# Kernel tuning notes

Hardware: AMD Instinct MI355X
Metric: run time of the kernel (lower is better)

The kernel has to match this reference:

```python
import jax, jax.numpy as jnp
import numpy as np
import math

INPUT_SIZE = 512
HIDDEN_SIZE = 1024
B, T = 64, 512


def setup_inputs() -> dict:
    key = jax.random.key(0)
    ks = jax.random.split(key, 8)
    stdv = 1.0 / math.sqrt(HIDDEN_SIZE)
    def U(k, shape):
        return jax.random.uniform(k, shape, jnp.float32, -stdv, stdv)
    x = jax.random.normal(ks[0], (B, T, INPUT_SIZE), jnp.float32)
    W_i_r = U(ks[1], (HIDDEN_SIZE, INPUT_SIZE))
    W_h_r = U(ks[2], (HIDDEN_SIZE, HIDDEN_SIZE))
    W_i_z = U(ks[3], (HIDDEN_SIZE, INPUT_SIZE))
    W_h_z = U(ks[4], (HIDDEN_SIZE, HIDDEN_SIZE))
    W_i_n = U(ks[5], (HIDDEN_SIZE, INPUT_SIZE))
    W_h_n = U(ks[6], (HIDDEN_SIZE, HIDDEN_SIZE))
    zeros = jnp.zeros((HIDDEN_SIZE,), jnp.float32)
    return {
        "x": x,
        "W_i_r": W_i_r, "b_i_r": zeros, "W_h_r": W_h_r, "b_h_r": zeros,
        "W_i_z": W_i_z, "b_i_z": zeros, "W_h_z": W_h_z, "b_h_z": zeros,
        "W_i_n": W_i_n, "b_i_n": zeros, "W_h_n": W_h_n, "b_h_n": zeros,
    }


def reference(x, W_i_r, b_i_r, W_h_r, b_h_r, W_i_z, b_i_z, W_h_z, b_h_z,
              W_i_n, b_i_n, W_h_n, b_h_n):
    Bn, Tn, _ = x.shape
    # Precompute all input projections in one batched matmul each: [B,T,H]
    xr = jnp.einsum('bti,hi->bth', x, W_i_r) + b_i_r
    xz = jnp.einsum('bti,hi->bth', x, W_i_z) + b_i_z
    xn = jnp.einsum('bti,hi->bth', x, W_i_n) + b_i_n

    h0 = jnp.zeros((Bn, W_h_r.shape[0]), x.dtype)

    def step(h, inp):
        xr_t, xz_t, xn_t = inp  # each [B,H]
        r = jax.nn.sigmoid(xr_t + h @ W_h_r.T + b_h_r)
        z = jax.nn.sigmoid(xz_t + h @ W_h_z.T + b_h_z)
        n = jnp.tanh(xn_t + r * (h @ W_h_n.T + b_h_n))
        h_new = (1.0 - z) * n + z * h
        return h_new, h_new

    # scan over time: inputs transposed to [T,B,H]
    xs = (xr.transpose(1, 0, 2), xz.transpose(1, 0, 2), xn.transpose(1, 0, 2))
    _, h_seq = jax.lax.scan(step, h0, xs)
    return h_seq.transpose(1, 0, 2)  # [B,T,H]
```

## Files before the change

### kernel.cpp

```cpp
#include <hip/hip_runtime.h>
#include <math.h>


#define BB 64
#define TT 512
#define II 512
#define HH 1024
#define JB 4
#define CK 128
#define PAD 132
#define XJ 16

__device__ __forceinline__ void fma4(float4& a, const float4 xv, const float4 w) {
    a.x += xv.x * w.x;
    a.y += xv.y * w.y;
    a.z += xv.z * w.z;
    a.w += xv.w * w.w;
}

__global__ __launch_bounds__(256) void xproj(
    const float* __restrict__ x,
    const float* __restrict__ Wir, const float* __restrict__ Wiz,
    const float* __restrict__ Win, float* __restrict__ xpre)
{
    __shared__ float xs[BB][PAD];
    const int tid  = threadIdx.x;
    const int b    = tid & 63;
    const int w    = tid >> 6;
    const int bid  = (int)blockIdx.x;
    const int t    = bid >> 6;
    const int jgrp = bid & 63;
    const int j0   = __builtin_amdgcn_readfirstlane(jgrp * XJ + w * 4);

    float4 acc[4][3];
#pragma unroll
    for (int jj = 0; jj < 4; ++jj)
#pragma unroll
        for (int g = 0; g < 3; ++g)
            acc[jj][g] = {0.f, 0.f, 0.f, 0.f};

    const float* xbase = x + (size_t)t * II;
    for (int kc = 0; kc < II / CK; ++kc) {
#pragma unroll
        for (int i = 0; i < 8; ++i) {
            int f   = tid + 256 * i;
            int row = f >> 5;
            int c4  = f & 31;
            *(float4*)&xs[row][c4 * 4] =
                *(const float4*)(xbase + (size_t)row * (TT * II) + kc * CK + c4 * 4);
        }
        __syncthreads();
        const float* xsrow = &xs[b][0];
#pragma unroll
        for (int k4 = 0; k4 < CK / 4; ++k4) {
            float4 xv = *(const float4*)(xsrow + k4 * 4);
#pragma unroll
            for (int jj = 0; jj < 4; ++jj) {
                const size_t wof = (size_t)(j0 + jj) * II + kc * CK + k4 * 4;
                fma4(acc[jj][0], xv, *(const float4*)(Wir + wof));
                fma4(acc[jj][1], xv, *(const float4*)(Wiz + wof));
                fma4(acc[jj][2], xv, *(const float4*)(Win + wof));
            }
        }
        __syncthreads();
    }

#pragma unroll
    for (int jj = 0; jj < 4; ++jj) {
        const int j = j0 + jj;
#pragma unroll
        for (int g = 0; g < 3; ++g) {
            float s = acc[jj][g].x + acc[jj][g].y + acc[jj][g].z + acc[jj][g].w;
            xpre[(((size_t)g * TT + t) * HH + j) * BB + b] = s;
        }
    }
}

__global__ __launch_bounds__(256) void gru_step_h(
    const float* __restrict__ Whr, const float* __restrict__ Whz,
    const float* __restrict__ Whn,
    const float* __restrict__ bir, const float* __restrict__ bhr,
    const float* __restrict__ biz, const float* __restrict__ bhz,
    const float* __restrict__ bin_, const float* __restrict__ bhn,
    const float* __restrict__ xpre,
    float* __restrict__ out, int t)
{
    __shared__ float xs[BB][PAD];
    const int tid = threadIdx.x;
    const int b   = tid & 63;
    const int jg  = tid >> 6;
    const int j   = __builtin_amdgcn_readfirstlane((int)blockIdx.x * JB + jg);

    const float bir_j = bir[j], bhr_j = bhr[j];
    const float biz_j = biz[j], bhz_j = bhz[j];
    const float bin_j = bin_[j], bhn_j = bhn[j];
    const float xr  = xpre[(((size_t)0 * TT + t) * HH + j) * BB + b];
    const float xz  = xpre[(((size_t)1 * TT + t) * HH + j) * BB + b];
    const float xn0 = xpre[(((size_t)2 * TT + t) * HH + j) * BB + b];
    float hprev = 0.f;
    if (t > 0)
        hprev = out[(size_t)b * (TT * HH) + (size_t)(t - 1) * HH + j];

    float4 aR  = {0.f, 0.f, 0.f, 0.f};
    float4 aZ  = {0.f, 0.f, 0.f, 0.f};
    float4 aHN = {0.f, 0.f, 0.f, 0.f};

    if (t > 0) {
        const float* hbase = out + (size_t)(t - 1) * HH;
        for (int kc = 0; kc < HH / CK; ++kc) {
#pragma unroll
            for (int i = 0; i < 8; ++i) {
                int f   = tid + 256 * i;
                int row = f >> 5;
                int c4  = f & 31;
                *(float4*)&xs[row][c4 * 4] =
                    *(const float4*)(hbase + (size_t)row * (TT * HH) + kc * CK + c4 * 4);
            }
            __syncthreads();
            const float* xsrow = &xs[b][0];
            const float* wr = Whr + (size_t)j * HH + kc * CK;
            const float* wz = Whz + (size_t)j * HH + kc * CK;
            const float* wn = Whn + (size_t)j * HH + kc * CK;
#pragma unroll
            for (int k4 = 0; k4 < CK / 4; ++k4) {
                float4 xv = *(const float4*)(xsrow + k4 * 4);
                fma4(aR,  xv, *(const float4*)(wr + k4 * 4));
                fma4(aZ,  xv, *(const float4*)(wz + k4 * 4));
                fma4(aHN, xv, *(const float4*)(wn + k4 * 4));
            }
            __syncthreads();
        }
    }

    float rpre = (aR.x + aR.y + aR.z + aR.w) + xr + bir_j + bhr_j;
    float zpre = (aZ.x + aZ.y + aZ.z + aZ.w) + xz + biz_j + bhz_j;
    float hn   = (aHN.x + aHN.y + aHN.z + aHN.w) + bhn_j;
    float xn   = xn0 + bin_j;

    float r = 1.f / (1.f + __expf(-rpre));
    float z = 1.f / (1.f + __expf(-zpre));
    float n = tanhf(xn + r * hn);

    out[(size_t)b * (TT * HH) + (size_t)t * HH + j] = (1.f - z) * n + z * hprev;
}

__device__ __forceinline__ void accum_chunk(
    const float* __restrict__ xsrow,
    const float* __restrict__ wr, const float* __restrict__ wz,
    const float* __restrict__ wn,
    float4& aR, float4& aZ, float4& aN)
{
#pragma unroll
    for (int k4 = 0; k4 < CK / 4; ++k4) {
        float4 xv = *(const float4*)(xsrow + k4 * 4);
        fma4(aR, xv, *(const float4*)(wr + k4 * 4));
        fma4(aZ, xv, *(const float4*)(wz + k4 * 4));
        fma4(aN, xv, *(const float4*)(wn + k4 * 4));
    }
}

__global__ __launch_bounds__(256) void gru_step_full(
    const float* __restrict__ x,
    const float* __restrict__ Wir, const float* __restrict__ Whr,
    const float* __restrict__ Wiz, const float* __restrict__ Whz,
    const float* __restrict__ Win, const float* __restrict__ Whn,
    const float* __restrict__ bir, const float* __restrict__ bhr,
    const float* __restrict__ biz, const float* __restrict__ bhz,
    const float* __restrict__ bin_, const float* __restrict__ bhn,
    float* __restrict__ out, int t)
{
    __shared__ float xs[BB][PAD];
    const int tid = threadIdx.x;
    const int b   = tid & 63;
    const int jg  = tid >> 6;
    const int j   = __builtin_amdgcn_readfirstlane((int)blockIdx.x * JB + jg);

    float4 aR  = {0.f, 0.f, 0.f, 0.f};
    float4 aZ  = {0.f, 0.f, 0.f, 0.f};
    float4 aXN = {0.f, 0.f, 0.f, 0.f};
    float4 aHN = {0.f, 0.f, 0.f, 0.f};

    const float* xbase = x + (size_t)t * II;
    for (int kc = 0; kc < II / CK; ++kc) {
#pragma unroll
        for (int i = 0; i < 8; ++i) {
            int f   = tid + 256 * i;
            int row = f >> 5;
            int c4  = f & 31;
            *(float4*)&xs[row][c4 * 4] =
                *(const float4*)(xbase + (size_t)row * (TT * II) + kc * CK + c4 * 4);
        }
        __syncthreads();
        accum_chunk(&xs[b][0],
                    Wir + (size_t)j * II + kc * CK,
                    Wiz + (size_t)j * II + kc * CK,
                    Win + (size_t)j * II + kc * CK,
                    aR, aZ, aXN);
        __syncthreads();
    }

    if (t > 0) {
        const float* hbase = out + (size_t)(t - 1) * HH;
        for (int kc = 0; kc < HH / CK; ++kc) {
#pragma unroll
            for (int i = 0; i < 8; ++i) {
                int f   = tid + 256 * i;
                int row = f >> 5;
                int c4  = f & 31;
                *(float4*)&xs[row][c4 * 4] =
                    *(const float4*)(hbase + (size_t)row * (TT * HH) + kc * CK + c4 * 4);
            }
            __syncthreads();
            accum_chunk(&xs[b][0],
                        Whr + (size_t)j * HH + kc * CK,
                        Whz + (size_t)j * HH + kc * CK,
                        Whn + (size_t)j * HH + kc * CK,
                        aR, aZ, aHN);
            __syncthreads();
        }
    }

    float rpre = (aR.x + aR.y + aR.z + aR.w) + bir[j] + bhr[j];
    float zpre = (aZ.x + aZ.y + aZ.z + aZ.w) + biz[j] + bhz[j];
    float hn   = (aHN.x + aHN.y + aHN.z + aHN.w) + bhn[j];
    float xn   = (aXN.x + aXN.y + aXN.z + aXN.w) + bin_[j];

    float r = 1.f / (1.f + __expf(-rpre));
    float z = 1.f / (1.f + __expf(-zpre));
    float n = tanhf(xn + r * hn);

    float hprev = (t > 0) ? out[(size_t)b * (TT * HH) + (size_t)(t - 1) * HH + j] : 0.f;
    out[(size_t)b * (TT * HH) + (size_t)t * HH + j] = (1.f - z) * n + z * hprev;
}

extern "C" void kernel_launch(void* const* d_in, const int* in_sizes, int n_in,
                              void* d_out, int out_size, void* d_ws, size_t ws_size,
                              hipStream_t stream) {
    (void)in_sizes; (void)n_in; (void)out_size;

    const float* x    = (const float*)d_in[0];
    const float* Wir  = (const float*)d_in[1];
    const float* bir  = (const float*)d_in[2];
    const float* Whr  = (const float*)d_in[3];
    const float* bhr  = (const float*)d_in[4];
    const float* Wiz  = (const float*)d_in[5];
    const float* biz  = (const float*)d_in[6];
    const float* Whz  = (const float*)d_in[7];
    const float* bhz  = (const float*)d_in[8];
    const float* Win  = (const float*)d_in[9];
    const float* bin_ = (const float*)d_in[10];
    const float* Whn  = (const float*)d_in[11];
    const float* bhn  = (const float*)d_in[12];
    float* out = (float*)d_out;

    const size_t need = (size_t)3 * TT * HH * BB * sizeof(float);
    if (d_ws != nullptr && ws_size >= need) {
        float* xpre = (float*)d_ws;
        xproj<<<dim3(TT * 64), dim3(256), 0, stream>>>(x, Wir, Wiz, Win, xpre);
        for (int t = 0; t < TT; ++t) {
            gru_step_h<<<dim3(HH / JB), dim3(256), 0, stream>>>(
                Whr, Whz, Whn, bir, bhr, biz, bhz, bin_, bhn, xpre, out, t);
        }
    } else {
        for (int t = 0; t < TT; ++t) {
            gru_step_full<<<dim3(HH / JB), dim3(256), 0, stream>>>(
                x, Wir, Whr, Wiz, Whz, Win, Whn,
                bir, bhr, biz, bhz, bin_, bhn, out, t);
        }
    }
}
```

Before: 15.86 ms.

## Replace per-timestep kernel launches with a persistent cooperative GRU kernel

Replaces the 512 per-timestep launches of gru_step_h with one cooperative persistent kernel of 256 blocks. Each block loops over time, keeps its biases in registers, reads the previous hidden state from a double-buffered packed global array, and synchronises all blocks through an atomic counter grid barrier after each step. This removes per-step kernel launch overhead. In exchange it adds the cost of a global barrier per step and relies on all blocks being co-resident; if the cooperative launch fails it falls back to the per-step launches.

Result: slower. 38.30 ms (+141.5%).

```diff
diff --git a/kernel.cpp b/kernel.cpp
--- a/kernel.cpp
+++ b/kernel.cpp
@@ -73,6 +73,103 @@
             float s = acc[jj][g].x + acc[jj][g].y + acc[jj][g].z + acc[jj][g].w;
             xpre[(((size_t)g * TT + t) * HH + j) * BB + b] = s;
         }
+    }
+}
+
+__global__ __launch_bounds__(256) void gru_persist(
+    const float* __restrict__ Whr, const float* __restrict__ Whz,
+    const float* __restrict__ Whn,
+    const float* __restrict__ bir, const float* __restrict__ bhr,
+    const float* __restrict__ biz, const float* __restrict__ bhz,
+    const float* __restrict__ bin_, const float* __restrict__ bhn,
+    const float* __restrict__ xpre,
+    float* __restrict__ out, float* __restrict__ hpack,
+    unsigned* __restrict__ bar)
+{
+    __shared__ float hs[CK * BB];
+    const int tid = threadIdx.x;
+    const int b   = tid & 63;
+    const int jg  = tid >> 6;
+    const int j   = __builtin_amdgcn_readfirstlane((int)blockIdx.x * JB + jg);
+
+    const float bir_j = bir[j], bhr_j = bhr[j];
+    const float biz_j = biz[j], bhz_j = bhz[j];
+    const float bin_j = bin_[j], bhn_j = bhn[j];
+
+    const size_t HB = (size_t)HH * BB;
+
+    for (int t = 0; t < TT; ++t) {
+        const float* hp_prev = hpack + (size_t)((t + 1) & 1) * HB;
+        float*       hp_cur  = hpack + (size_t)(t & 1) * HB;
+
+        const float xr  = xpre[(((size_t)0 * TT + t) * HH + j) * BB + b];
+        const float xz  = xpre[(((size_t)1 * TT + t) * HH + j) * BB + b];
+        const float xn0 = xpre[(((size_t)2 * TT + t) * HH + j) * BB + b];
+
+        float4 aR  = {0.f, 0.f, 0.f, 0.f};
+        float4 aZ  = {0.f, 0.f, 0.f, 0.f};
+        float4 aHN = {0.f, 0.f, 0.f, 0.f};
+        float hprev = 0.f;
+
+        if (t > 0) {
+            hprev = hp_prev[(size_t)j * BB + b];
+#pragma unroll 1
+            for (int kc = 0; kc < HH / CK; ++kc) {
+                const float* src = hp_prev + (size_t)kc * (CK * BB);
+#pragma unroll
+                for (int i = 0; i < 8; ++i) {
+                    const int f = tid + 256 * i;
+                    *(float4*)&hs[f * 4] = *(const float4*)(src + (size_t)f * 4);
+                }
+                __syncthreads();
+                const float* wr = Whr + (size_t)j * HH + kc * CK;
+                const float* wz = Whz + (size_t)j * HH + kc * CK;
+                const float* wn = Whn + (size_t)j * HH + kc * CK;
+#pragma unroll
+                for (int k4 = 0; k4 < CK / 4; ++k4) {
+                    const float4 wrv = *(const float4*)(wr + k4 * 4);
+                    const float4 wzv = *(const float4*)(wz + k4 * 4);
+                    const float4 wnv = *(const float4*)(wn + k4 * 4);
+                    const float h0 = hs[(k4 * 4 + 0) * 64 + b];
+                    const float h1 = hs[(k4 * 4 + 1) * 64 + b];
+                    const float h2 = hs[(k4 * 4 + 2) * 64 + b];
+                    const float h3 = hs[(k4 * 4 + 3) * 64 + b];
+                    aR.x  += h0 * wrv.x; aR.y  += h1 * wrv.y;
+                    aR.z  += h2 * wrv.z; aR.w  += h3 * wrv.w;
+                    aZ.x  += h0 * wzv.x; aZ.y  += h1 * wzv.y;
+                    aZ.z  += h2 * wzv.z; aZ.w  += h3 * wzv.w;
+                    aHN.x += h0 * wnv.x; aHN.y += h1 * wnv.y;
+                    aHN.z += h2 * wnv.z; aHN.w += h3 * wnv.w;
+                }
+                __syncthreads();
+            }
+        }
+
+        float rpre = (aR.x + aR.y + aR.z + aR.w) + xr + bir_j + bhr_j;
+        float zpre = (aZ.x + aZ.y + aZ.z + aZ.w) + xz + biz_j + bhz_j;
+        float hn   = (aHN.x + aHN.y + aHN.z + aHN.w) + bhn_j;
+        float xn   = xn0 + bin_j;
+
+        float r = 1.f / (1.f + __expf(-rpre));
+        float z = 1.f / (1.f + __expf(-zpre));
+        float n = tanhf(xn + r * hn);
+        float hnew = (1.f - z) * n + z * hprev;
+
+        out[(size_t)b * (TT * HH) + (size_t)t * HH + j] = hnew;
+        hp_cur[(size_t)j * BB + b] = hnew;
+
+        __syncthreads();
+        if (tid == 0) {
+            __threadfence();
+            __hip_atomic_fetch_add(bar, 1u, __ATOMIC_RELAXED,
+                                   __HIP_MEMORY_SCOPE_AGENT);
+            const unsigned tgt = 256u * (unsigned)(t + 1);
+            while (__hip_atomic_load(bar, __ATOMIC_RELAXED,
+                                     __HIP_MEMORY_SCOPE_AGENT) < tgt)
+                __builtin_amdgcn_s_sleep(2);
+            __threadfence();
+        }
+        __syncthreads();
     }
 }
 
@@ -253,13 +350,30 @@
     const float* bhn  = (const float*)d_in[12];
     float* out = (float*)d_out;
 
-    const size_t need = (size_t)3 * TT * HH * BB * sizeof(float);
+    const size_t XPRE_BYTES  = (size_t)3 * TT * HH * BB * sizeof(float);
+    const size_t HPACK_BYTES = (size_t)2 * HH * BB * sizeof(float);
+    const size_t need = XPRE_BYTES + HPACK_BYTES + 256;
+
     if (d_ws != nullptr && ws_size >= need) {
-        float* xpre = (float*)d_ws;
+        float*    xpre  = (float*)d_ws;
+        float*    hpack = (float*)((char*)d_ws + XPRE_BYTES);
+        unsigned* bar   = (unsigned*)((char*)d_ws + XPRE_BYTES + HPACK_BYTES);
+
+        hipMemsetAsync(bar, 0, 64, stream);
         xproj<<<dim3(TT * 64), dim3(256), 0, stream>>>(x, Wir, Wiz, Win, xpre);
-        for (int t = 0; t < TT; ++t) {
-            gru_step_h<<<dim3(HH / JB), dim3(256), 0, stream>>>(
-                Whr, Whz, Whn, bir, bhr, biz, bhz, bin_, bhn, xpre, out, t);
+
+        void* args[] = { (void*)&Whr, (void*)&Whz, (void*)&Whn,
+                         (void*)&bir, (void*)&bhr, (void*)&biz, (void*)&bhz,
+                         (void*)&bin_, (void*)&bhn, (void*)&xpre,
+                         (void*)&out, (void*)&hpack, (void*)&bar };
+        hipError_t e = hipLaunchCooperativeKernel((const void*)gru_persist,
+                                                  dim3(256), dim3(256),
+                                                  args, 0, stream);
+        if (e != hipSuccess) {
+            for (int t = 0; t < TT; ++t) {
+                gru_step_h<<<dim3(HH / JB), dim3(256), 0, stream>>>(
+                    Whr, Whz, Whn, bir, bhr, biz, bhz, bin_, bhn, xpre, out, t);
+            }
         }
     } else {
         for (int t = 0; t < TT; ++t) {
```
